# Kernel tuning notes

Hardware: AMD Instinct MI355X
Metric: run time of the kernel (lower is better)

Reference implementation:

```python
import jax, jax.numpy as jnp
import numpy as np

N, P, DM, E, NNZ = 30000, 8, 128, 1000, 120000
DIN = P * DM
EPS = 1e-5


def setup_inputs():
    key = jax.random.key(0)
    ks = jax.random.split(key, 12)

    def nrm(k, shp, s=0.02):
        return jax.random.normal(k, shp, dtype=jnp.float32) * s

    node_idx = jax.random.randint(ks[0], (NNZ,), 0, N)
    # ensure max edge id == E-1 so num_edges = max+1 semantics hold
    edge_idx = jax.random.randint(ks[1], (NNZ,), 0, E).at[0].set(E - 1)
    return dict(
        x=jax.random.normal(ks[2], (N, P, DM), dtype=jnp.float32),
        node_idx=node_idx, edge_idx=edge_idx, num_edges=E,
        W1=nrm(ks[3], (DIN, DM)), b1=jnp.zeros((DM,), jnp.float32),
        bn1_g=jnp.ones((DM,), jnp.float32), bn1_b=jnp.zeros((DM,), jnp.float32),
        h1_lin=nrm(ks[4], (DM, 4 * DM)), h1_att=nrm(ks[5], (4, 2 * DM), 0.1),
        h1_bias=jnp.zeros((DM,), jnp.float32),
        bn2_g=jnp.ones((DM,), jnp.float32), bn2_b=jnp.zeros((DM,), jnp.float32),
        h2_lin=nrm(ks[6], (DM, DM)), h2_att=nrm(ks[7], (1, 2 * DM), 0.1),
        h2_bias=jnp.zeros((DM,), jnp.float32),
        bn3_g=jnp.ones((DM,), jnp.float32), bn3_b=jnp.zeros((DM,), jnp.float32),
        W2=nrm(ks[8], (DM, DIN)), b2=jnp.zeros((DIN,), jnp.float32),
        bn4_g=jnp.ones((DM,), jnp.float32), bn4_b=jnp.zeros((DM,), jnp.float32),
    )


def _bn(x, g, b, axes):
    # train-mode BatchNorm (batch statistics, biased variance, eps=1e-5)
    m = x.mean(axes, keepdims=True)
    v = x.var(axes, keepdims=True)
    return (x - m) * jax.lax.rsqrt(v + EPS) * g + b


def _hconv(x, v_idx, e_idx, hw, he_attr, lin_w, att, bias, heads, n, e):
    # PyG HypergraphConv, use_attention=True, attention_mode='node', concat=False
    d = lin_w.shape[1] // heads
    xh = (x @ lin_w).reshape(n, heads, d)           # [N, H, D]
    eh = (he_attr @ lin_w).reshape(e, heads, d)     # [E, H, D]
    alpha = (xh[v_idx] * att[None, :, :d]).sum(-1) + (eh[e_idx] * att[None, :, d:]).sum(-1)
    alpha = jax.nn.leaky_relu(alpha, 0.2)           # [nnz, H]
    amax = jax.ops.segment_max(alpha, e_idx, num_segments=e)
    ex = jnp.exp(alpha - amax[e_idx])
    alpha = ex / (jax.ops.segment_sum(ex, e_idx, num_segments=e)[e_idx] + 1e-16)
    D = jax.ops.segment_sum(hw[e_idx], v_idx, num_segments=n)
    Dinv = jnp.where(D > 0, 1.0 / D, 0.0)
    B = jax.ops.segment_sum(jnp.ones((v_idx.shape[0],), x.dtype), e_idx, num_segments=e)
    Binv = jnp.where(B > 0, 1.0 / B, 0.0)
    # node -> edge
    m1 = Binv[e_idx][:, None, None] * xh[v_idx] * alpha[:, :, None]
    out_e = jax.ops.segment_sum(m1, e_idx, num_segments=e)
    # edge -> node
    m2 = Dinv[v_idx][:, None, None] * out_e[e_idx] * alpha[:, :, None]
    out = jax.ops.segment_sum(m2, v_idx, num_segments=n)
    return out.mean(1) + bias


def reference(x, node_idx, edge_idx, num_edges, W1, b1, bn1_g, bn1_b,
              h1_lin, h1_att, h1_bias, bn2_g, bn2_b, h2_lin, h2_att, h2_bias,
              bn3_g, bn3_b, W2, b2, bn4_g, bn4_b):
    src = x
    n = x.shape[0]
    h = x.reshape(n, -1)
    h = jax.nn.leaky_relu(h @ W1 + b1, 0.2)
    h = _bn(h, bn1_g, bn1_b, 0)
    # dense incidence (to_dense_adj equivalent, sliced to [:, :num_edges])
    a = jnp.zeros((n, num_edges), h.dtype).at[node_idx, edge_idx].add(1.0)
    hw = jnp.ones((num_edges,), h.dtype)
    he_attr = a.T @ h
    h = h + _hconv(h, node_idx, edge_idx, hw, he_attr, h1_lin, h1_att, h1_bias, 4, n, num_edges)
    h = _bn(h, bn2_g, bn2_b, 0)
    he_attr = a.T @ h
    h = h + _hconv(h, node_idx, edge_idx, hw, he_attr, h2_lin, h2_att, h2_bias, 1, n, num_edges)
    h = _bn(h, bn3_g, bn3_b, 0)
    h = jax.nn.leaky_relu(h @ W2 + b2, 0.2)
    out = src + h.reshape(n, -1, DM)
    # bn4 = Transpose->BatchNorm1d(d_model)->Transpose: normalize per channel over (N, P)
    out = _bn(out, bn4_g[None, None, :], bn4_b[None, None, :], (0, 1))
    return out
```

## Files before the change

kernel.cpp:

```cpp
#include <hip/hip_runtime.h>
#include <math.h>

#define NN 30000
#define PP 8
#define DM 128
#define EE 1000
#define NNZC 120000
#define DIN (PP*DM)

typedef __attribute__((ext_vector_type(8))) short bf16x8;
typedef __attribute__((ext_vector_type(4))) float f32x4;

__device__ __forceinline__ short f2bf(float f) {
    union { float f; unsigned u; } v; v.f = f;
    unsigned r = v.u + 0x7fffu + ((v.u >> 16) & 1u);
    return (short)(r >> 16);
}
__device__ __forceinline__ float bf2f(short s) {
    union { unsigned u; float f; } v;
    v.u = ((unsigned)(unsigned short)s) << 16;
    return v.f;
}

__global__ void count_kernel(const int* __restrict__ ei, const int* __restrict__ ni,
                             int* __restrict__ ecnt, int* __restrict__ ncnt) {
    int k = blockIdx.x * 256 + threadIdx.x;
    if (k >= NNZC) return;
    atomicAdd(&ecnt[ei[k]], 1);
    atomicAdd(&ncnt[ni[k]], 1);
}

__global__ __launch_bounds__(1024)
void scan_two(const int* __restrict__ ecnt, int* __restrict__ eoff,
              const int* __restrict__ ncnt, int* __restrict__ noff) {
    const int* cnt; int* off; int len;
    if (blockIdx.x == 0) { cnt = ecnt; off = eoff; len = EE; }
    else                 { cnt = ncnt; off = noff; len = NN; }
    __shared__ int wsum[16];
    __shared__ int carrysh;
    int t = threadIdx.x;
    int lane = t & 63, w = t >> 6;
    if (t == 0) carrysh = 0;
    __syncthreads();
    for (int base = 0; base < len; base += 1024) {
        int v = (base + t < len) ? cnt[base + t] : 0;
        int s = v;
        #pragma unroll
        for (int d = 1; d < 64; d <<= 1) {
            int u = __shfl_up(s, d);
            if (lane >= d) s += u;
        }
        if (lane == 63) wsum[w] = s;
        __syncthreads();
        if (t < 16) {
            int ws = wsum[t];
            #pragma unroll
            for (int d = 1; d < 16; d <<= 1) {
                int u = __shfl_up(ws, d);
                if (t >= d) ws += u;
            }
            wsum[t] = ws;
        }
        __syncthreads();
        int c = carrysh;
        int woff = (w > 0) ? wsum[w - 1] : 0;
        if (base + t < len) off[base + t] = c + woff + s - v;
        int total = wsum[15];
        __syncthreads();
        if (t == 0) carrysh = c + total;
    }
    __syncthreads();
    if (t == 0) off[len] = carrysh;
}

__global__ void fill_lists(const int* __restrict__ ei, const int* __restrict__ ni,
                           const int* __restrict__ eoff, const int* __restrict__ noff,
                           int* __restrict__ ecur, int* __restrict__ ncur,
                           int* __restrict__ elist, int* __restrict__ nlist) {
    int k = blockIdx.x * 256 + threadIdx.x;
    if (k >= NNZC) return;
    int e = ei[k];
    int p = atomicAdd(&ecur[e], 1);
    elist[eoff[e] + p] = k;
    int n = ni[k];
    int q = atomicAdd(&ncur[n], 1);
    nlist[noff[n] + q] = k;
}

__global__ void transpose_to_bf16(const float* __restrict__ B, short* __restrict__ BT,
                                  int K, int N) {
    __shared__ float tile[32][33];
    int bn = blockIdx.x * 32, bk = blockIdx.y * 32;
    int tx = threadIdx.x & 31, ty = threadIdx.x >> 5;
    #pragma unroll
    for (int yy = ty; yy < 32; yy += 8) {
        int k = bk + yy, n = bn + tx;
        tile[yy][tx] = (k < K && n < N) ? B[(size_t)k * N + n] : 0.f;
    }
    __syncthreads();
    #pragma unroll
    for (int yy = ty; yy < 32; yy += 8) {
        int n = bn + yy, k = bk + tx;
        if (n < N && k < K) BT[(size_t)n * K + k] = f2bf(tile[tx][yy]);
    }
}

__global__ __launch_bounds__(256)
void gemm1_splitk(const float* __restrict__ x, const short* __restrict__ W1T,
                  float* __restrict__ hp, short* __restrict__ xb) {
    __shared__ short As[64 * 40];
    __shared__ short Bs[128 * 40];
    const int tid = threadIdx.x;
    const int lane = tid & 63, wid = tid >> 6;
    const int wm = wid >> 1, wn = wid & 1;
    const int panel = blockIdx.x >> 1, khalf = blockIdx.x & 1;
    const int row0 = panel * 64;
    const int kbase = khalf * 512;
    const int srow = tid >> 2, skq = tid & 3;

    f32x4 acc[2][4] = {};
    struct Stage { float4 fa[2]; bf16x8 b[2]; };
    Stage s0, s1;

    auto loadT = [&](int t, Stage& s) {
        int k0 = kbase + (t << 5);
        int gr = row0 + srow;
        float4 z = make_float4(0.f, 0.f, 0.f, 0.f);
        s.fa[0] = z; s.fa[1] = z;
        if (gr < NN) {
            const float4* p = (const float4*)(x + (size_t)gr * DIN + k0 + skq * 8);
            s.fa[0] = p[0]; s.fa[1] = p[1];
        }
        #pragma unroll
        for (int c = 0; c < 2; ++c)
            s.b[c] = *(const bf16x8*)(W1T + (size_t)(srow + 64 * c) * DIN + k0 + skq * 8);
    };
    auto writeT = [&](int t, Stage& s) {
        int k0 = kbase + (t << 5);
        bf16x8 t8;
        t8[0] = f2bf(s.fa[0].x); t8[1] = f2bf(s.fa[0].y);
        t8[2] = f2bf(s.fa[0].z); t8[3] = f2bf(s.fa[0].w);
        t8[4] = f2bf(s.fa[1].x); t8[5] = f2bf(s.fa[1].y);
        t8[6] = f2bf(s.fa[1].z); t8[7] = f2bf(s.fa[1].w);
        int gr = row0 + srow;
        if (gr < NN)
            *(bf16x8*)(xb + (size_t)gr * DIN + k0 + skq * 8) = t8;
        *(bf16x8*)&As[srow * 40 + skq * 8] = t8;
        #pragma unroll
        for (int c = 0; c < 2; ++c)
            *(bf16x8*)&Bs[(srow + 64 * c) * 40 + skq * 8] = s.b[c];
    };
    auto compute = [&]() {
        bf16x8 av[2], bv[4];
        #pragma unroll
        for (int i = 0; i < 2; ++i)
            av[i] = *(const bf16x8*)&As[(wm * 32 + i * 16 + (lane & 15)) * 40 + (lane >> 4) * 8];
        #pragma unroll
        for (int j = 0; j < 4; ++j)
            bv[j] = *(const bf16x8*)&Bs[(wn * 64 + j * 16 + (lane & 15)) * 40 + (lane >> 4) * 8];
        #pragma unroll
        for (int i = 0; i < 2; ++i)
            #pragma unroll
            for (int j = 0; j < 4; ++j)
                acc[i][j] = __builtin_amdgcn_mfma_f32_16x16x32_bf16(av[i], bv[j], acc[i][j], 0, 0, 0);
    };

    loadT(0, s0);
    for (int t = 0; t < 16; t += 2) {
        __syncthreads();
        loadT(t + 1, s1);
        writeT(t, s0);
        __syncthreads();
        compute();
        __syncthreads();
        if (t + 2 < 16) loadT(t + 2, s0);
        writeT(t + 1, s1);
        __syncthreads();
        compute();
    }

    float* o = hp + (size_t)khalf * NN * 128;
    #pragma unroll
    for (int i = 0; i < 2; ++i) {
        #pragma unroll
        for (int q = 0; q < 4; ++q) {
            int row = row0 + wm * 32 + i * 16 + (lane >> 4) * 4 + q;
            if (row < NN) {
                #pragma unroll
                for (int j = 0; j < 4; ++j) {
                    int col = wn * 64 + j * 16 + (lane & 15);
                    o[(size_t)row * 128 + col] = acc[i][j][q];
                }
            }
        }
    }
}

__global__ void combine_bn1(const float* __restrict__ hp, const float* __restrict__ b1,
                            float* __restrict__ h, float* __restrict__ spart) {
    int t = threadIdx.x;
    const float4* p0 = (const float4*)hp;
    const float4* p1 = (const float4*)(hp + (size_t)NN * 128);
    float4* o = (float4*)h;
    int c = (t & 31) * 4;
    float4 bb = *(const float4*)(b1 + c);
    long long idx = (long long)blockIdx.x * 256 + t;
    long long stride = (long long)gridDim.x * 256;
    float s1[4] = {0.f,0.f,0.f,0.f}, s2[4] = {0.f,0.f,0.f,0.f};
    for (; idx < (long long)NN * 32; idx += stride) {
        float4 a = p0[idx], b = p1[idx];
        float v0 = a.x + b.x + bb.x; v0 = v0 > 0.f ? v0 : 0.2f * v0;
        float v1 = a.y + b.y + bb.y; v1 = v1 > 0.f ? v1 : 0.2f * v1;
        float v2 = a.z + b.z + bb.z; v2 = v2 > 0.f ? v2 : 0.2f * v2;
        float v3 = a.w + b.w + bb.w; v3 = v3 > 0.f ? v3 : 0.2f * v3;
        o[idx] = make_float4(v0, v1, v2, v3);
        s1[0] += v0; s2[0] += v0 * v0;
        s1[1] += v1; s2[1] += v1 * v1;
        s1[2] += v2; s2[2] += v2 * v2;
        s1[3] += v3; s2[3] += v3 * v3;
    }
    __shared__ float r1[256][4], r2[256][4];
    #pragma unroll
    for (int k = 0; k < 4; ++k) { r1[t][k] = s1[k]; r2[t][k] = s2[k]; }
    __syncthreads();
    if (t < 32) {
        #pragma unroll
        for (int k = 0; k < 4; ++k) {
            float a1 = 0.f, a2 = 0.f;
            #pragma unroll
            for (int u = 0; u < 8; ++u) { a1 += r1[t + u * 32][k]; a2 += r2[t + u * 32][k]; }
            spart[(size_t)blockIdx.x * 256 + t * 4 + k] = a1;
            spart[(size_t)blockIdx.x * 256 + 128 + t * 4 + k] = a2;
        }
    }
}

template<int RG, bool HASBIAS, bool LEAKY, bool ADDSRC, bool STATS, bool OUTBF16, bool SWZ>
__global__ __launch_bounds__(256)
void gemm_mfma(const short* __restrict__ Ain, const short* __restrict__ BT,
               const float* __restrict__ bias, const short* __restrict__ srcb,
               void* __restrict__ Cout, float* __restrict__ spart,
               int M, int K, int Nc, int colB) {
    constexpr int BM = 64 * RG;
    __shared__ short As[BM * 40];
    __shared__ short Bs[128 * 40];
    const int tid = threadIdx.x;
    const int lane = tid & 63, wid = tid >> 6;
    const int wm = wid >> 1, wn = wid & 1;

    int row0, col0;
    {
        int w = blockIdx.x;
        int l;
        if (SWZ) { int cpx = gridDim.x >> 3; l = (w & 7) * cpx + (w >> 3); }
        else     { l = w; }
        row0 = (l / colB) * BM;
        col0 = (l % colB) * 128;
    }
    const int srow = tid >> 2, skq = tid & 3;

    f32x4 acc[RG * 2][4] = {};
    const int NT = K >> 5;

    struct Stage { bf16x8 a[RG]; bf16x8 b[2]; };
    Stage s0, s1;

    auto loadT = [&](int t, Stage& s) {
        int k0 = t << 5;
        #pragma unroll
        for (int c = 0; c < RG; ++c) {
            int gr = row0 + srow + 64 * c;
            s.a[c] = bf16x8{0, 0, 0, 0, 0, 0, 0, 0};
            if (gr < M)
                s.a[c] = *(const bf16x8*)(Ain + (size_t)gr * K + k0 + skq * 8);
        }
        #pragma unroll
        for (int c = 0; c < 2; ++c) {
            int gc = col0 + srow + 64 * c;
            s.b[c] = *(const bf16x8*)(BT + (size_t)gc * K + k0 + skq * 8);
        }
    };
    auto writeT = [&](Stage& s) {
        #pragma unroll
        for (int c = 0; c < RG; ++c)
            *(bf16x8*)&As[(srow + 64 * c) * 40 + skq * 8] = s.a[c];
        #pragma unroll
        for (int c = 0; c < 2; ++c)
            *(bf16x8*)&Bs[(srow + 64 * c) * 40 + skq * 8] = s.b[c];
    };
    auto compute = [&]() {
        bf16x8 av[RG * 2], bv[4];
        #pragma unroll
        for (int i = 0; i < RG * 2; ++i)
            av[i] = *(const bf16x8*)&As[(wm * (RG * 32) + i * 16 + (lane & 15)) * 40 + (lane >> 4) * 8];
        #pragma unroll
        for (int j = 0; j < 4; ++j)
            bv[j] = *(const bf16x8*)&Bs[(wn * 64 + j * 16 + (lane & 15)) * 40 + (lane >> 4) * 8];
        #pragma unroll
        for (int i = 0; i < RG * 2; ++i)
            #pragma unroll
            for (int j = 0; j < 4; ++j)
                acc[i][j] = __builtin_amdgcn_mfma_f32_16x16x32_bf16(av[i], bv[j], acc[i][j], 0, 0, 0);
    };

    loadT(0, s0);
    for (int t = 0; t < NT; t += 2) {
        __syncthreads();
        loadT(t + 1, s1);
        writeT(s0);
        __syncthreads();
        compute();
        __syncthreads();
        if (t + 2 < NT) loadT(t + 2, s0);
        writeT(s1);
        __syncthreads();
        compute();
    }

    float* Cf = (float*)Cout;
    short* Cb = (short*)Cout;
    float lsum[4] = {0.f, 0.f, 0.f, 0.f}, lsq[4] = {0.f, 0.f, 0.f, 0.f};
    #pragma unroll
    for (int i = 0; i < RG * 2; ++i) {
        #pragma unroll
        for (int q = 0; q < 4; ++q) {
            int row = row0 + wm * (RG * 32) + i * 16 + (lane >> 4) * 4 + q;
            if (row < M) {
                #pragma unroll
                for (int j = 0; j < 4; ++j) {
                    int col = col0 + wn * 64 + j * 16 + (lane & 15);
                    float val = acc[i][j][q];
                    if (HASBIAS) val += bias[col];
                    if (LEAKY)   val = val > 0.f ? val : 0.2f * val;
                    if (ADDSRC)  val += bf2f(srcb[(size_t)row * Nc + col]);
                    if (STATS) { lsum[j] += val; lsq[j] += val * val; }
                    if (OUTBF16) Cb[(size_t)row * Nc + col] = f2bf(val);
                    else         Cf[(size_t)row * Nc + col] = val;
                }
            }
        }
    }
    if (STATS) {
        __syncthreads();
        float* sred = (float*)As;
        sred[tid] = 0.f;
        __syncthreads();
        int ch = wn * 64 + (lane & 15);
        #pragma unroll
        for (int j = 0; j < 4; ++j) {
            atomicAdd(&sred[ch + j * 16], lsum[j]);
            atomicAdd(&sred[128 + ch + j * 16], lsq[j]);
        }
        __syncthreads();
        spart[(size_t)blockIdx.x * 256 + tid] = sred[tid];
    }
}

__global__ void reduce_stats(const float* __restrict__ part, int nblk, float* __restrict__ accum) {
    int t = threadIdx.x;
    float s = 0.f;
    for (int b = blockIdx.x; b < nblk; b += gridDim.x)
        s += part[(size_t)b * 256 + t];
    atomicAdd(&accum[t], s);
}

template<bool SHADOW>
__global__ void bn_apply_f(float* __restrict__ a, short* __restrict__ shadow, long long total4,
                           const float* __restrict__ accum, const float* __restrict__ g,
                           const float* __restrict__ b, float invM) {
    __shared__ float scs[256];
    int t = threadIdx.x;
    if (t < 128) {
        float mean = accum[t] * invM;
        float var = accum[128 + t] * invM - mean * mean;
        float s = g[t] * rsqrtf(var + 1e-5f);
        scs[t] = s;
        scs[128 + t] = b[t] - mean * s;
    }
    __syncthreads();
    long long idx = (long long)blockIdx.x * 256 + t;
    long long stride = (long long)gridDim.x * 256;
    float4* a4 = (float4*)a;
    short4* s4p = (short4*)shadow;
    for (; idx < total4; idx += stride) {
        int c = (int)((idx & 31) * 4);
        float4 v = a4[idx];
        v.x = v.x * scs[c + 0] + scs[128 + c + 0];
        v.y = v.y * scs[c + 1] + scs[128 + c + 1];
        v.z = v.z * scs[c + 2] + scs[128 + c + 2];
        v.w = v.w * scs[c + 3] + scs[128 + c + 3];
        a4[idx] = v;
        if (SHADOW)
            s4p[idx] = make_short4(f2bf(v.x), f2bf(v.y), f2bf(v.z), f2bf(v.w));
    }
}

__global__ void bn_apply_b2f(const short* __restrict__ inb, float* __restrict__ outp,
                             long long total4, const float* __restrict__ accum,
                             const float* __restrict__ g, const float* __restrict__ b, float invM) {
    __shared__ float scs[256];
    int t = threadIdx.x;
    if (t < 128) {
        float mean = accum[t] * invM;
        float var = accum[128 + t] * invM - mean * mean;
        float s = g[t] * rsqrtf(var + 1e-5f);
        scs[t] = s;
        scs[128 + t] = b[t] - mean * s;
    }
    __syncthreads();
    long long idx = (long long)blockIdx.x * 256 + t;
    long long stride = (long long)gridDim.x * 256;
    const short4* in4 = (const short4*)inb;
    float4* o4 = (float4*)outp;
    for (; idx < total4; idx += stride) {
        int c = (int)((idx & 31) * 4);
        short4 sv = in4[idx];
        float4 v;
        v.x = bf2f(sv.x) * scs[c + 0] + scs[128 + c + 0];
        v.y = bf2f(sv.y) * scs[c + 1] + scs[128 + c + 1];
        v.z = bf2f(sv.z) * scs[c + 2] + scs[128 + c + 2];
        v.w = bf2f(sv.w) * scs[c + 3] + scs[128 + c + 3];
        o4[idx] = v;
    }
}

__global__ void edge_feat(const int* __restrict__ elist, const int* __restrict__ eoff,
                          const int* __restrict__ nidx, const float* __restrict__ h,
                          float* __restrict__ he) {
    __shared__ int nIdx[128];
    int e = blockIdx.x;
    int off = eoff[e], cnt = eoff[e + 1] - off;
    int d = threadIdx.x;
    float acc = 0.f;
    for (int base = 0; base < cnt; base += 128) {
        int c = cnt - base; if (c > 128) c = 128;
        if (d < c) nIdx[d] = nidx[elist[off + base + d]];
        __syncthreads();
        #pragma unroll 4
        for (int j = 0; j < c; ++j)
            acc += h[(size_t)nIdx[j] * 128 + d];
        __syncthreads();
    }
    he[(size_t)e * 128 + d] = acc;
}

template<int H>
__global__ void watt_kernel(const float* __restrict__ lin, const float* __restrict__ att,
                            float* __restrict__ wx, float* __restrict__ we) {
    int t = threadIdx.x;
    int hh = t >> 7, d = t & 127;
    float sx = 0.f, se = 0.f;
    for (int j = 0; j < 128; ++j) {
        float l = lin[(size_t)d * (H * 128) + hh * 128 + j];
        sx += l * att[hh * 256 + j];
        se += l * att[hh * 256 + 128 + j];
    }
    wx[t] = sx;
    we[t] = se;
}

template<int H>
__global__ void dots128(const float* __restrict__ feat, const float* __restrict__ w,
                        float* __restrict__ out, int M) {
    int wv = threadIdx.x >> 6;
    int lane = threadIdx.x & 63;
    int row = blockIdx.x * 4 + wv;
    if (row >= M) return;
    const float* fr = feat + (size_t)row * 128;
    float f0 = fr[lane], f1 = fr[lane + 64];
    #pragma unroll
    for (int h = 0; h < H; ++h) {
        float v = f0 * w[h * 128 + lane] + f1 * w[h * 128 + lane + 64];
        #pragma unroll
        for (int s = 32; s > 0; s >>= 1) v += __shfl_xor(v, s);
        if (lane == 0) out[(size_t)row * H + h] = v;
    }
}

template<int H>
__global__ void edge_softmax(const int* __restrict__ elist, const int* __restrict__ eoff,
                             const int* __restrict__ nidx, const float* __restrict__ ax,
                             const float* __restrict__ ae, float* __restrict__ alpha) {
    constexpr int SLOTS = 256 / H;
    __shared__ float red[256];
    int e = blockIdx.x;
    int off = eoff[e], cnt = eoff[e + 1] - off;
    int t = threadIdx.x;
    int h = t % H, slot = t / H;
    float aeh = ae[(size_t)e * H + h];
    float lmax = -1e30f;
    for (int p = slot; p < cnt; p += SLOTS) {
        int k = elist[off + p];
        int n = nidx[k];
        float v = ax[(size_t)n * H + h] + aeh;
        v = v > 0.f ? v : 0.2f * v;
        alpha[(size_t)k * H + h] = v;
        lmax = fmaxf(lmax, v);
    }
    red[t] = lmax;
    __syncthreads();
    for (int s = SLOTS / 2; s > 0; s >>= 1) {
        if (slot < s) red[slot * H + h] = fmaxf(red[slot * H + h], red[(slot + s) * H + h]);
        __syncthreads();
    }
    float m = red[h];
    __syncthreads();
    float lsum = 0.f;
    for (int p = slot; p < cnt; p += SLOTS) {
        int k = elist[off + p];
        float ex = expf(alpha[(size_t)k * H + h] - m);
        alpha[(size_t)k * H + h] = ex;
        lsum += ex;
    }
    red[t] = lsum;
    __syncthreads();
    for (int s = SLOTS / 2; s > 0; s >>= 1) {
        if (slot < s) red[slot * H + h] += red[(slot + s) * H + h];
        __syncthreads();
    }
    float inv = 1.0f / (red[h] + 1e-16f);
    for (int p = slot; p < cnt; p += SLOTS) {
        int k = elist[off + p];
        alpha[(size_t)k * H + h] *= inv;
    }
}

template<int H>
__global__ void edge_agg128(const int* __restrict__ elist, const int* __restrict__ eoff,
                            const int* __restrict__ nidx, const float* __restrict__ alpha,
                            const float* __restrict__ h, float* __restrict__ agg) {
    __shared__ int nIdx[128];
    __shared__ float aBuf[128 * H];
    int e = blockIdx.x;
    int off = eoff[e], cnt = eoff[e + 1] - off;
    int t = threadIdx.x;
    int hh = t >> 7, d = t & 127;
    float acc = 0.f;
    for (int base = 0; base < cnt; base += 128) {
        int c = cnt - base; if (c > 128) c = 128;
        if (t < c) {
            int k = elist[off + base + t];
            nIdx[t] = nidx[k];
            if (H == 4) {
                float4 a4 = *(const float4*)(alpha + (size_t)k * 4);
                aBuf[t * 4 + 0] = a4.x; aBuf[t * 4 + 1] = a4.y;
                aBuf[t * 4 + 2] = a4.z; aBuf[t * 4 + 3] = a4.w;
            } else {
                aBuf[t] = alpha[k];
            }
        }
        __syncthreads();
        #pragma unroll 4
        for (int j = 0; j < c; ++j)
            acc += aBuf[j * H + hh] * h[(size_t)nIdx[j] * 128 + d];
        __syncthreads();
    }
    float binv = cnt > 0 ? 1.0f / (float)cnt : 0.0f;
    agg[(size_t)e * (H * 128) + t] = acc * binv;
}

template<int H>
__global__ void oute_lin(const float* __restrict__ agg, const float* __restrict__ lin,
                         float* __restrict__ oute) {
    __shared__ float ar[H * 128];
    int e = blockIdx.x;
    int t = threadIdx.x;
    ar[t] = agg[(size_t)e * (H * 128) + t];
    __syncthreads();
    int hh = t >> 7;
    float acc = 0.f;
    #pragma unroll 4
    for (int d = 0; d < 128; ++d)
        acc += ar[hh * 128 + d] * lin[(size_t)d * (H * 128) + t];
    oute[(size_t)e * (H * 128) + t] = acc;
}

template<int H>
__global__ __launch_bounds__(256)
void node_aggregate2(const int* __restrict__ nlist, const int* __restrict__ noff,
                     const int* __restrict__ eidx, const float* __restrict__ alpha,
                     const float* __restrict__ oute, const float* __restrict__ bias,
                     float* __restrict__ hout, float* __restrict__ spart) {
    constexpr int MAXM = 32;
    __shared__ int   eLDS[2][MAXM];
    __shared__ float aLDS[2][MAXM][H];
    __shared__ float red[256];
    __shared__ int cshare[2];
    const int tid = threadIdx.x;
    const int sub = tid >> 7, d = tid & 127;
    const float bd = bias[d];
    float sts = 0.f, stq = 0.f;
    for (int sweep = 0; sweep < 8; ++sweep) {
        int n = sweep * 3750 + blockIdx.x * 2 + sub;
        int off = noff[n], cnt = noff[n + 1] - off;
        if (d == 0) cshare[sub] = cnt;
        __syncthreads();
        int cmax = max(cshare[0], cshare[1]);
        float acc[H];
        #pragma unroll
        for (int hh = 0; hh < H; ++hh) acc[hh] = 0.f;
        for (int base = 0; base < cmax; base += MAXM) {
            int chunkN = cnt - base;
            if (chunkN > MAXM) chunkN = MAXM;
            if (d < chunkN) {
                int k = nlist[off + base + d];
                eLDS[sub][d] = eidx[k];
                if (H == 4) {
                    float4 a4 = *(const float4*)(alpha + (size_t)k * 4);
                    aLDS[sub][d][0] = a4.x; aLDS[sub][d][1] = a4.y;
                    aLDS[sub][d][2] = a4.z; aLDS[sub][d][3] = a4.w;
                } else {
                    aLDS[sub][d][0] = alpha[k];
                }
            }
            __syncthreads();
            for (int j = 0; j < chunkN; ++j) {
                int e = eLDS[sub][j];
                #pragma unroll
                for (int hh = 0; hh < H; ++hh)
                    acc[hh] += aLDS[sub][j][hh] * oute[(size_t)e * (H * 128) + hh * 128 + d];
            }
            __syncthreads();
        }
        float s = 0.f;
        #pragma unroll
        for (int hh = 0; hh < H; ++hh) s += acc[hh];
        float dinv = cnt > 0 ? 1.0f / (float)cnt : 0.f;
        float nv = hout[(size_t)n * 128 + d] + s * (1.0f / H) * dinv + bd;
        hout[(size_t)n * 128 + d] = nv;
        sts += nv; stq += nv * nv;
        __syncthreads();
    }
    red[tid] = sts;
    __syncthreads();
    float tsum = (sub == 0) ? red[d] + red[128 + d] : 0.f;
    __syncthreads();
    red[tid] = stq;
    __syncthreads();
    if (sub == 0) {
        spart[(size_t)blockIdx.x * 256 + d] = tsum;
        spart[(size_t)blockIdx.x * 256 + 128 + d] = red[d] + red[128 + d];
    }
}

extern "C" void kernel_launch(void* const* d_in, const int* in_sizes, int n_in,
                              void* d_out, int out_size, void* d_ws, size_t ws_size,
                              hipStream_t stream) {
    (void)in_sizes; (void)n_in; (void)out_size; (void)ws_size;
    const float* x        = (const float*)d_in[0];
    const int*   node_idx = (const int*)d_in[1];
    const int*   edge_idx = (const int*)d_in[2];
    const float* W1    = (const float*)d_in[4];
    const float* b1    = (const float*)d_in[5];
    const float* bn1_g = (const float*)d_in[6];
    const float* bn1_b = (const float*)d_in[7];
    const float* h1_lin  = (const float*)d_in[8];
    const float* h1_att  = (const float*)d_in[9];
    const float* h1_bias = (const float*)d_in[10];
    const float* bn2_g = (const float*)d_in[11];
    const float* bn2_b = (const float*)d_in[12];
    const float* h2_lin  = (const float*)d_in[13];
    const float* h2_att  = (const float*)d_in[14];
    const float* h2_bias = (const float*)d_in[15];
    const float* bn3_g = (const float*)d_in[16];
    const float* bn3_b = (const float*)d_in[17];
    const float* W2    = (const float*)d_in[18];
    const float* b2    = (const float*)d_in[19];
    const float* bn4_g = (const float*)d_in[20];
    const float* bn4_b = (const float*)d_in[21];
    float* out = (float*)d_out;

    char* ws = (char*)d_ws;
    size_t off = 0;
    auto alloc = [&](size_t bytes) -> void* {
        void* p = ws + off;
        off = (off + bytes + 255) & ~(size_t)255;
        return p;
    };
    float* h     = (float*)alloc((size_t)NN * 128 * 4);
    float* scratch = (float*)alloc((size_t)NN * 512 * 4);
    float* he    = (float*)alloc((size_t)EE * 128 * 4);
    float* agg   = (float*)alloc((size_t)EE * 512 * 4);
    float* oute  = (float*)alloc((size_t)EE * 512 * 4);
    float* ax    = (float*)alloc((size_t)NN * 4 * 4);
    float* ae    = (float*)alloc((size_t)EE * 4 * 4);
    float* alpha = (float*)alloc((size_t)NNZC * 4 * 4);
    float* accum = (float*)alloc(256 * 4);
    float* spart = (float*)alloc((size_t)1880 * 256 * 4);
    float* wax   = (float*)alloc(512 * 4);
    float* wae   = (float*)alloc(512 * 4);
    short* hb    = (short*)alloc((size_t)NN * 128 * 2);
    short* W1T   = (short*)alloc((size_t)128 * DIN * 2);
    short* W2T   = (short*)alloc((size_t)DIN * 128 * 2);
    int* ecnt  = (int*)alloc(EE * 4);
    int* eoff  = (int*)alloc((EE + 1) * 4);
    int* ecur  = (int*)alloc(EE * 4);
    int* elist = (int*)alloc(NNZC * 4);
    int* ncnt  = (int*)alloc(NN * 4);
    int* noff  = (int*)alloc((NN + 1) * 4);
    int* ncur  = (int*)alloc(NN * 4);
    int* nlist = (int*)alloc(NNZC * 4);

    short* xb   = (short*)d_out;
    float* hp   = scratch;
    short* outb = (short*)scratch;

    hipMemsetAsync(ecnt, 0, EE * 4, stream);
    hipMemsetAsync(ncnt, 0, NN * 4, stream);
    hipMemsetAsync(ecur, 0, EE * 4, stream);
    hipMemsetAsync(ncur, 0, NN * 4, stream);

    count_kernel<<<(NNZC + 255) / 256, 256, 0, stream>>>(edge_idx, node_idx, ecnt, ncnt);
    transpose_to_bf16<<<dim3(4, 32), 256, 0, stream>>>(W1, W1T, DIN, 128);
    transpose_to_bf16<<<dim3(32, 4), 256, 0, stream>>>(W2, W2T, 128, DIN);
    scan_two<<<2, 1024, 0, stream>>>(ecnt, eoff, ncnt, noff);
    fill_lists<<<(NNZC + 255) / 256, 256, 0, stream>>>(edge_idx, node_idx, eoff, noff,
                                                       ecur, ncur, elist, nlist);

    const int MB64  = (NN + 63) / 64;
    const int MB128 = (NN + 127) / 128;

    gemm1_splitk<<<2 * MB64, 256, 0, stream>>>(x, W1T, hp, xb);
    hipMemsetAsync(accum, 0, 256 * 4, stream);
    combine_bn1<<<1024, 256, 0, stream>>>(hp, b1, h, spart);
    reduce_stats<<<32, 256, 0, stream>>>(spart, 1024, accum);
    bn_apply_f<false><<<1024, 256, 0, stream>>>(h, nullptr, (long long)NN * 128 / 4, accum,
                                                bn1_g, bn1_b, 1.0f / NN);

    edge_feat<<<EE, 128, 0, stream>>>(elist, eoff, node_idx, h, he);
    watt_kernel<4><<<1, 512, 0, stream>>>(h1_lin, h1_att, wax, wae);
    dots128<4><<<(NN + 3) / 4, 256, 0, stream>>>(h, wax, ax, NN);
    dots128<4><<<(EE + 3) / 4, 256, 0, stream>>>(he, wae, ae, EE);
    edge_softmax<4><<<EE, 256, 0, stream>>>(elist, eoff, node_idx, ax, ae, alpha);
    edge_agg128<4><<<EE, 512, 0, stream>>>(elist, eoff, node_idx, alpha, h, agg);
    oute_lin<4><<<EE, 512, 0, stream>>>(agg, h1_lin, oute);
    node_aggregate2<4><<<1875, 256, 0, stream>>>(nlist, noff, edge_idx, alpha, oute, h1_bias,
                                                 h, spart);

    hipMemsetAsync(accum, 0, 256 * 4, stream);
    reduce_stats<<<32, 256, 0, stream>>>(spart, 1875, accum);
    bn_apply_f<false><<<1024, 256, 0, stream>>>(h, nullptr, (long long)NN * 128 / 4, accum,
                                                bn2_g, bn2_b, 1.0f / NN);

    edge_feat<<<EE, 128, 0, stream>>>(elist, eoff, node_idx, h, he);
    watt_kernel<1><<<1, 128, 0, stream>>>(h2_lin, h2_att, wax, wae);
    dots128<1><<<(NN + 3) / 4, 256, 0, stream>>>(h, wax, ax, NN);
    dots128<1><<<(EE + 3) / 4, 256, 0, stream>>>(he, wae, ae, EE);
    edge_softmax<1><<<EE, 256, 0, stream>>>(elist, eoff, node_idx, ax, ae, alpha);
    edge_agg128<1><<<EE, 128, 0, stream>>>(elist, eoff, node_idx, alpha, h, agg);
    oute_lin<1><<<EE, 128, 0, stream>>>(agg, h2_lin, oute);
    node_aggregate2<1><<<1875, 256, 0, stream>>>(nlist, noff, edge_idx, alpha, oute, h2_bias,
                                                 h, spart);

    hipMemsetAsync(accum, 0, 256 * 4, stream);
    reduce_stats<<<32, 256, 0, stream>>>(spart, 1875, accum);
    bn_apply_f<true><<<1024, 256, 0, stream>>>(h, hb, (long long)NN * 128 / 4, accum,
                                               bn3_g, bn3_b, 1.0f / NN);

    hipMemsetAsync(accum, 0, 256 * 4, stream);
    gemm_mfma<2, true, true, true, true, true, true>
        <<<8 * MB128, 256, 0, stream>>>(hb, W2T, b2, xb, outb, spart, NN, 128, DIN, 8);
    reduce_stats<<<32, 256, 0, stream>>>(spart, 8 * MB128, accum);

    bn_apply_b2f<<<2048, 256, 0, stream>>>(outb, out, (long long)NN * DIN / 4, accum,
                                           bn4_g, bn4_b, 1.0f / (NN * PP));
}
```

Measured before the change: 583.1 us.

## Split-K gemm1 four ways, drop bf16 x copy, project edge attention linearly

Three changes in one. The first GEMM is split into four K-quarters instead of two, with the combine kernel summing four partials. The bf16 copy of x is no longer written, and the final GEMM adds the fp32 x residual directly, which also removes bf16 rounding from the residual. Edge features are no longer gathered at full 128-dim width. Because the projection is linear, per-node attention dots against the edge weights are computed once and summed per edge, replacing edge_feat and a second dots pass. This trades more partial-buffer traffic in the combine step for removing the xb write and the wide edge gathers.

```diff
diff --git a/kernel.cpp b/kernel.cpp
--- a/kernel.cpp
+++ b/kernel.cpp
@@ -107,15 +107,15 @@
 
 __global__ __launch_bounds__(256)
 void gemm1_splitk(const float* __restrict__ x, const short* __restrict__ W1T,
-                  float* __restrict__ hp, short* __restrict__ xb) {
+                  float* __restrict__ hp) {
     __shared__ short As[64 * 40];
     __shared__ short Bs[128 * 40];
     const int tid = threadIdx.x;
     const int lane = tid & 63, wid = tid >> 6;
     const int wm = wid >> 1, wn = wid & 1;
-    const int panel = blockIdx.x >> 1, khalf = blockIdx.x & 1;
+    const int panel = blockIdx.x >> 2, kq = blockIdx.x & 3;
     const int row0 = panel * 64;
-    const int kbase = khalf * 512;
+    const int kbase = kq * 256;
     const int srow = tid >> 2, skq = tid & 3;
 
     f32x4 acc[2][4] = {};
@@ -135,16 +135,12 @@
         for (int c = 0; c < 2; ++c)
             s.b[c] = *(const bf16x8*)(W1T + (size_t)(srow + 64 * c) * DIN + k0 + skq * 8);
     };
-    auto writeT = [&](int t, Stage& s) {
-        int k0 = kbase + (t << 5);
+    auto writeT = [&](Stage& s) {
         bf16x8 t8;
         t8[0] = f2bf(s.fa[0].x); t8[1] = f2bf(s.fa[0].y);
         t8[2] = f2bf(s.fa[0].z); t8[3] = f2bf(s.fa[0].w);
         t8[4] = f2bf(s.fa[1].x); t8[5] = f2bf(s.fa[1].y);
         t8[6] = f2bf(s.fa[1].z); t8[7] = f2bf(s.fa[1].w);
-        int gr = row0 + srow;
-        if (gr < NN)
-            *(bf16x8*)(xb + (size_t)gr * DIN + k0 + skq * 8) = t8;
         *(bf16x8*)&As[srow * 40 + skq * 8] = t8;
         #pragma unroll
         for (int c = 0; c < 2; ++c)
@@ -166,20 +162,20 @@
     };
 
     loadT(0, s0);
-    for (int t = 0; t < 16; t += 2) {
+    for (int t = 0; t < 8; t += 2) {
         __syncthreads();
         loadT(t + 1, s1);
-        writeT(t, s0);
+        writeT(s0);
         __syncthreads();
         compute();
         __syncthreads();
-        if (t + 2 < 16) loadT(t + 2, s0);
-        writeT(t + 1, s1);
+        if (t + 2 < 8) loadT(t + 2, s0);
+        writeT(s1);
         __syncthreads();
         compute();
     }
 
-    float* o = hp + (size_t)khalf * NN * 128;
+    float* o = hp + (size_t)kq * NN * 128;
     #pragma unroll
     for (int i = 0; i < 2; ++i) {
         #pragma unroll
@@ -201,6 +197,8 @@
     int t = threadIdx.x;
     const float4* p0 = (const float4*)hp;
     const float4* p1 = (const float4*)(hp + (size_t)NN * 128);
+    const float4* p2 = (const float4*)(hp + (size_t)2 * NN * 128);
+    const float4* p3 = (const float4*)(hp + (size_t)3 * NN * 128);
     float4* o = (float4*)h;
     int c = (t & 31) * 4;
     float4 bb = *(const float4*)(b1 + c);
@@ -208,11 +206,11 @@
     long long stride = (long long)gridDim.x * 256;
     float s1[4] = {0.f,0.f,0.f,0.f}, s2[4] = {0.f,0.f,0.f,0.f};
     for (; idx < (long long)NN * 32; idx += stride) {
-        float4 a = p0[idx], b = p1[idx];
-        float v0 = a.x + b.x + bb.x; v0 = v0 > 0.f ? v0 : 0.2f * v0;
-        float v1 = a.y + b.y + bb.y; v1 = v1 > 0.f ? v1 : 0.2f * v1;
-        float v2 = a.z + b.z + bb.z; v2 = v2 > 0.f ? v2 : 0.2f * v2;
-        float v3 = a.w + b.w + bb.w; v3 = v3 > 0.f ? v3 : 0.2f * v3;
+        float4 a = p0[idx], b = p1[idx], cc = p2[idx], dd = p3[idx];
+        float v0 = a.x + b.x + cc.x + dd.x + bb.x; v0 = v0 > 0.f ? v0 : 0.2f * v0;
+        float v1 = a.y + b.y + cc.y + dd.y + bb.y; v1 = v1 > 0.f ? v1 : 0.2f * v1;
+        float v2 = a.z + b.z + cc.z + dd.z + bb.z; v2 = v2 > 0.f ? v2 : 0.2f * v2;
+        float v3 = a.w + b.w + cc.w + dd.w + bb.w; v3 = v3 > 0.f ? v3 : 0.2f * v3;
         o[idx] = make_float4(v0, v1, v2, v3);
         s1[0] += v0; s2[0] += v0 * v0;
         s1[1] += v1; s2[1] += v1 * v1;
@@ -238,7 +236,7 @@
 template<int RG, bool HASBIAS, bool LEAKY, bool ADDSRC, bool STATS, bool OUTBF16, bool SWZ>
 __global__ __launch_bounds__(256)
 void gemm_mfma(const short* __restrict__ Ain, const short* __restrict__ BT,
-               const float* __restrict__ bias, const short* __restrict__ srcb,
+               const float* __restrict__ bias, const float* __restrict__ srcf,
                void* __restrict__ Cout, float* __restrict__ spart,
                int M, int K, int Nc, int colB) {
     constexpr int BM = 64 * RG;
@@ -332,7 +330,7 @@
                     float val = acc[i][j][q];
                     if (HASBIAS) val += bias[col];
                     if (LEAKY)   val = val > 0.f ? val : 0.2f * val;
-                    if (ADDSRC)  val += bf2f(srcb[(size_t)row * Nc + col]);
+                    if (ADDSRC)  val += srcf[(size_t)row * Nc + col];
                     if (STATS) { lsum[j] += val; lsq[j] += val * val; }
                     if (OUTBF16) Cb[(size_t)row * Nc + col] = f2bf(val);
                     else         Cf[(size_t)row * Nc + col] = val;
@@ -424,26 +422,6 @@
     }
 }
 
-__global__ void edge_feat(const int* __restrict__ elist, const int* __restrict__ eoff,
-                          const int* __restrict__ nidx, const float* __restrict__ h,
-                          float* __restrict__ he) {
-    __shared__ int nIdx[128];
-    int e = blockIdx.x;
-    int off = eoff[e], cnt = eoff[e + 1] - off;
-    int d = threadIdx.x;
-    float acc = 0.f;
-    for (int base = 0; base < cnt; base += 128) {
-        int c = cnt - base; if (c > 128) c = 128;
-        if (d < c) nIdx[d] = nidx[elist[off + base + d]];
-        __syncthreads();
-        #pragma unroll 4
-        for (int j = 0; j < c; ++j)
-            acc += h[(size_t)nIdx[j] * 128 + d];
-        __syncthreads();
-    }
-    he[(size_t)e * 128 + d] = acc;
-}
-
 template<int H>
 __global__ void watt_kernel(const float* __restrict__ lin, const float* __restrict__ att,
                             float* __restrict__ wx, float* __restrict__ we) {
@@ -460,8 +438,9 @@
 }
 
 template<int H>
-__global__ void dots128(const float* __restrict__ feat, const float* __restrict__ w,
-                        float* __restrict__ out, int M) {
+__global__ void dots128_2(const float* __restrict__ feat, const float* __restrict__ wx,
+                          const float* __restrict__ we, float* __restrict__ oax,
+                          float* __restrict__ oaxe, int M) {
     int wv = threadIdx.x >> 6;
     int lane = threadIdx.x & 63;
     int row = blockIdx.x * 4 + wv;
@@ -470,11 +449,44 @@
     float f0 = fr[lane], f1 = fr[lane + 64];
     #pragma unroll
     for (int h = 0; h < H; ++h) {
-        float v = f0 * w[h * 128 + lane] + f1 * w[h * 128 + lane + 64];
-        #pragma unroll
-        for (int s = 32; s > 0; s >>= 1) v += __shfl_xor(v, s);
-        if (lane == 0) out[(size_t)row * H + h] = v;
-    }
+        float va = f0 * wx[h * 128 + lane] + f1 * wx[h * 128 + lane + 64];
+        float vb = f0 * we[h * 128 + lane] + f1 * we[h * 128 + lane + 64];
+        #pragma unroll
+        for (int s = 32; s > 0; s >>= 1) { va += __shfl_xor(va, s); vb += __shfl_xor(vb, s); }
+        if (lane == 0) {
+            oax[(size_t)row * H + h] = va;
+            oaxe[(size_t)row * H + h] = vb;
+        }
+    }
+}
+
+template<int H>
+__global__ void edge_sum_ae(const int* __restrict__ elist, const int* __restrict__ eoff,
+                            const int* __restrict__ nidx, const float* __restrict__ axe,
+                            float* __restrict__ ae) {
+    __shared__ float red[4 * 128];
+    int e = blockIdx.x;
+    int off = eoff[e], cnt = eoff[e + 1] - off;
+    int t = threadIdx.x;
+    float acc[H];
+    #pragma unroll
+    for (int hh = 0; hh < H; ++hh) acc[hh] = 0.f;
+    for (int p = t; p < cnt; p += 128) {
+        int n = nidx[elist[off + p]];
+        #pragma unroll
+        for (int hh = 0; hh < H; ++hh) acc[hh] += axe[(size_t)n * H + hh];
+    }
+    #pragma unroll
+    for (int hh = 0; hh < H; ++hh) red[hh * 128 + t] = acc[hh];
+    __syncthreads();
+    for (int s = 64; s > 0; s >>= 1) {
+        if (t < s) {
+            #pragma unroll
+            for (int hh = 0; hh < H; ++hh) red[hh * 128 + t] += red[hh * 128 + t + s];
+        }
+        __syncthreads();
+    }
+    if (t < H) ae[(size_t)e * H + t] = red[t * 128];
 }
 
 template<int H>
@@ -679,10 +691,10 @@
     };
     float* h     = (float*)alloc((size_t)NN * 128 * 4);
     float* scratch = (float*)alloc((size_t)NN * 512 * 4);
-    float* he    = (float*)alloc((size_t)EE * 128 * 4);
     float* agg   = (float*)alloc((size_t)EE * 512 * 4);
     float* oute  = (float*)alloc((size_t)EE * 512 * 4);
     float* ax    = (float*)alloc((size_t)NN * 4 * 4);
+    float* axe   = (float*)alloc((size_t)NN * 4 * 4);
     float* ae    = (float*)alloc((size_t)EE * 4 * 4);
     float* alpha = (float*)alloc((size_t)NNZC * 4 * 4);
     float* accum = (float*)alloc(256 * 4);
@@ -701,7 +713,6 @@
     int* ncur  = (int*)alloc(NN * 4);
     int* nlist = (int*)alloc(NNZC * 4);
 
-    short* xb   = (short*)d_out;
     float* hp   = scratch;
     short* outb = (short*)scratch;
 
@@ -720,17 +731,16 @@
     const int MB64  = (NN + 63) / 64;
     const int MB128 = (NN + 127) / 128;
 
-    gemm1_splitk<<<2 * MB64, 256, 0, stream>>>(x, W1T, hp, xb);
+    gemm1_splitk<<<4 * MB64, 256, 0, stream>>>(x, W1T, hp);
     hipMemsetAsync(accum, 0, 256 * 4, stream);
     combine_bn1<<<1024, 256, 0, stream>>>(hp, b1, h, spart);
     reduce_stats<<<32, 256, 0, stream>>>(spart, 1024, accum);
     bn_apply_f<false><<<1024, 256, 0, stream>>>(h, nullptr, (long long)NN * 128 / 4, accum,
                                                 bn1_g, bn1_b, 1.0f / NN);
 
-    edge_feat<<<EE, 128, 0, stream>>>(elist, eoff, node_idx, h, he);
     watt_kernel<4><<<1, 512, 0, stream>>>(h1_lin, h1_att, wax, wae);
-    dots128<4><<<(NN + 3) / 4, 256, 0, stream>>>(h, wax, ax, NN);
-    dots128<4><<<(EE + 3) / 4, 256, 0, stream>>>(he, wae, ae, EE);
+    dots128_2<4><<<(NN + 3) / 4, 256, 0, stream>>>(h, wax, wae, ax, axe, NN);
+    edge_sum_ae<4><<<EE, 128, 0, stream>>>(elist, eoff, node_idx, axe, ae);
     edge_softmax<4><<<EE, 256, 0, stream>>>(elist, eoff, node_idx, ax, ae, alpha);
     edge_agg128<4><<<EE, 512, 0, stream>>>(elist, eoff, node_idx, alpha, h, agg);
     oute_lin<4><<<EE, 512, 0, stream>>>(agg, h1_lin, oute);
@@ -742,10 +752,9 @@
     bn_apply_f<false><<<1024, 256, 0, stream>>>(h, nullptr, (long long)NN * 128 / 4, accum,
                                                 bn2_g, bn2_b, 1.0f / NN);
 
-    edge_feat<<<EE, 128, 0, stream>>>(elist, eoff, node_idx, h, he);
     watt_kernel<1><<<1, 128, 0, stream>>>(h2_lin, h2_att, wax, wae);
-    dots128<1><<<(NN + 3) / 4, 256, 0, stream>>>(h, wax, ax, NN);
-    dots128<1><<<(EE + 3) / 4, 256, 0, stream>>>(he, wae, ae, EE);
+    dots128_2<1><<<(NN + 3) / 4, 256, 0, stream>>>(h, wax, wae, ax, axe, NN);
+    edge_sum_ae<1><<<EE, 128, 0, stream>>>(elist, eoff, node_idx, axe, ae);
     edge_softmax<1><<<EE, 256, 0, stream>>>(elist, eoff, node_idx, ax, ae, alpha);
     edge_agg128<1><<<EE, 128, 0, stream>>>(elist, eoff, node_idx, alpha, h, agg);
     oute_lin<1><<<EE, 128, 0, stream>>>(agg, h2_lin, oute);
@@ -759,7 +768,7 @@
 
     hipMemsetAsync(accum, 0, 256 * 4, stream);
     gemm_mfma<2, true, true, true, true, true, true>
-        <<<8 * MB128, 256, 0, stream>>>(hb, W2T, b2, xb, outb, spart, NN, 128, DIN, 8);
+        <<<8 * MB128, 256, 0, stream>>>(hb, W2T, b2, x, outb, spart, NN, 128, DIN, 8);
     reduce_stats<<<32, 256, 0, stream>>>(spart, 8 * MB128, accum);
 
     bn_apply_b2f<<<2048, 256, 0, stream>>>(outb, out, (long long)NN * DIN / 4, accum,
```

Measured after the change: 540.0 us. 7.4% less time.
